# Optimization experiments

Measured on AMD Instinct MI355X. Metric: run time of the kernel, lower is better.

The kernel has to match this reference:

```python
import jax, jax.numpy as jnp
import numpy as np

NUM_LAYER = 6
NUM_HEADS = 1
NEG_INF = -1e9


def setup_inputs() -> dict:
    key = jax.random.key(0)
    ks = jax.random.split(key, 8)
    bs, C, N = 8, 128, 2048
    H0 = (jax.random.uniform(ks[0], (bs, N, N)) < 0.2).astype(jnp.float32)
    vertex_feat = jax.random.normal(ks[1], (bs, C, N), dtype=jnp.float32)
    edge_feat = jax.random.normal(ks[2], (bs, C, N), dtype=jnp.float32)
    s = 1.0 / np.sqrt(C)  # Conv1d(k=1) default init scale
    Wq = jax.random.uniform(ks[3], (C, C), minval=-s, maxval=s, dtype=jnp.float32)
    bq = jax.random.uniform(ks[4], (C,), minval=-s, maxval=s, dtype=jnp.float32)
    Wk = jax.random.uniform(ks[5], (C, C), minval=-s, maxval=s, dtype=jnp.float32)
    bk = jax.random.uniform(ks[6], (C,), minval=-s, maxval=s, dtype=jnp.float32)
    return {"H0": H0, "vertex_feat": vertex_feat, "edge_feat": edge_feat,
            "Wq": Wq, "bq": bq, "Wk": Wk, "bk": bk, "it": 4}


def reference(H0, vertex_feat, edge_feat, Wq, bq, Wk, bk, it):
    bs, N, _ = H0.shape
    C = Wq.shape[0]
    head = NUM_HEADS
    dh = C // head
    # Conv1d kernel_size=1 == pointwise linear over channel dim
    Q = (jnp.einsum('oc,bcn->bon', Wq, vertex_feat) + bq[None, :, None]).reshape(bs, head, dh, N)
    K = (jnp.einsum('oc,bcn->bon', Wk, edge_feat) + bk[None, :, None]).reshape(bs, head, dh, N)
    att = jnp.einsum('bhco,bhci->bhoi', Q, K) / np.sqrt(dh)  # [bs,h,N,N]
    mask = jnp.where(H0 > 0, 0.0, NEG_INF)                   # masked_fill(1-H0)
    score = jax.nn.sigmoid(att + mask[:, None]).sum(axis=1) / head  # [bs,N,N]
    # mask_score, choice='topk': keep top-k scores per row
    k = round(N * 0.1 * (NUM_LAYER - 1 - it))
    topk_vals = jax.lax.top_k(score, k)[0]          # [bs,N,k]
    a_min = topk_vals[..., -1:]                     # k-th largest per row
    W = jnp.where(score >= a_min, score, 0.0)
    H = jnp.where(W > 0, H0, 0.0)
    # degree-normalization matrices (diag_embed of 1/deg, inf -> 0)
    deg_E = H.sum(axis=1)   # [bs,N] edge degrees
    deg_V = H.sum(axis=2)   # [bs,N] vertex degrees
    De_n_1 = jax.vmap(jnp.diag)(jnp.where(deg_E != 0, 1.0 / deg_E, 0.0))
    Dv_n_1 = jax.vmap(jnp.diag)(jnp.where(deg_V != 0, 1.0 / deg_V, 0.0))
    # edge weights: L2-normalized column sums of W (F.normalize, eps=1e-12)
    W_edge = W.sum(axis=1)
    nrm = jnp.maximum(jnp.linalg.norm(W_edge, axis=1, keepdims=True), 1e-12)
    W_edge = (W_edge / nrm)[:, :, None]  # [bs,N,1]
    return H, W, De_n_1, Dv_n_1, W_edge
```

## Files before the change

kernel.cpp:

```cpp
#include <hip/hip_runtime.h>
#include <math.h>

#define NUM_LAYER 6

__global__ __launch_bounds__(256) void qk_gemm(
    const float* __restrict__ Wq, const float* __restrict__ bq,
    const float* __restrict__ vf,
    const float* __restrict__ Wk, const float* __restrict__ bk,
    const float* __restrict__ ef,
    float* __restrict__ Qout, float* __restrict__ Kout,
    int C, int N, int bs) {
  int which = (int)blockIdx.y >= bs;
  int b = (int)blockIdx.y - (which ? bs : 0);
  const float* Wm = which ? Wk : Wq;
  const float* bias = which ? bk : bq;
  const float* X = (which ? ef : vf) + (size_t)b * C * N;
  float* P = (which ? Kout : Qout) + (size_t)b * C * N;
  int n0 = blockIdx.x * 128;
  __shared__ float As[8][128];
  __shared__ float Xs[8][128];
  int t = threadIdx.x;
  int tx = t & 15, ty = t >> 4;
  int ao = t >> 1, ac = (t & 1) * 4;
  int lk = t >> 5, lj = (t & 31) * 4;
  float acc[8][8] = {};
  for (int c0 = 0; c0 < C; c0 += 8) {
    __syncthreads();
    float4 wv = *(const float4*)&Wm[(size_t)ao * C + c0 + ac];
    As[ac + 0][ao] = wv.x; As[ac + 1][ao] = wv.y;
    As[ac + 2][ao] = wv.z; As[ac + 3][ao] = wv.w;
    *(float4*)&Xs[lk][lj] = *(const float4*)&X[(size_t)(c0 + lk) * N + n0 + lj];
    __syncthreads();
#pragma unroll
    for (int kk = 0; kk < 8; ++kk) {
      float a[8], bb[8];
      *(float4*)&a[0]  = *(const float4*)&As[kk][ty * 4];
      *(float4*)&a[4]  = *(const float4*)&As[kk][64 + ty * 4];
      *(float4*)&bb[0] = *(const float4*)&Xs[kk][tx * 4];
      *(float4*)&bb[4] = *(const float4*)&Xs[kk][64 + tx * 4];
#pragma unroll
      for (int i = 0; i < 8; ++i)
#pragma unroll
        for (int j = 0; j < 8; ++j)
          acc[i][j] = fmaf(a[i], bb[j], acc[i][j]);
    }
  }
#pragma unroll
  for (int i = 0; i < 8; ++i) {
    int row = (i >> 2) * 64 + ty * 4 + (i & 3);
    float bv = bias[row];
    float4 o0 = { acc[i][0] + bv, acc[i][1] + bv, acc[i][2] + bv, acc[i][3] + bv };
    float4 o1 = { acc[i][4] + bv, acc[i][5] + bv, acc[i][6] + bv, acc[i][7] + bv };
    *(float4*)&P[(size_t)row * N + n0 + tx * 4] = o0;
    *(float4*)&P[(size_t)row * N + n0 + 64 + tx * 4] = o1;
  }
}

__global__ __launch_bounds__(256) void att_score(
    const float* __restrict__ Q, const float* __restrict__ K,
    const float* __restrict__ H0, float* __restrict__ score,
    int C, int N, float rsdh) {
  int b = blockIdx.z;
  int o0 = blockIdx.y * 128, i0 = blockIdx.x * 128;
  const float* Qb = Q + (size_t)b * C * N;
  const float* Kb = K + (size_t)b * C * N;
  const float* Hb = H0 + (size_t)b * N * N;
  float* Sb = score + (size_t)b * N * N;
  __shared__ float As[8][128];
  __shared__ float Bs[8][128];
  int t = threadIdx.x;
  int tx = t & 15, ty = t >> 4;
  int lk = t >> 5, lj = (t & 31) * 4;
  float acc[8][8] = {};
  for (int c0 = 0; c0 < C; c0 += 8) {
    __syncthreads();
    *(float4*)&As[lk][lj] = *(const float4*)&Qb[(size_t)(c0 + lk) * N + o0 + lj];
    *(float4*)&Bs[lk][lj] = *(const float4*)&Kb[(size_t)(c0 + lk) * N + i0 + lj];
    __syncthreads();
#pragma unroll
    for (int kk = 0; kk < 8; ++kk) {
      float a[8], bb[8];
      *(float4*)&a[0]  = *(const float4*)&As[kk][ty * 4];
      *(float4*)&a[4]  = *(const float4*)&As[kk][64 + ty * 4];
      *(float4*)&bb[0] = *(const float4*)&Bs[kk][tx * 4];
      *(float4*)&bb[4] = *(const float4*)&Bs[kk][64 + tx * 4];
#pragma unroll
      for (int i = 0; i < 8; ++i)
#pragma unroll
        for (int j = 0; j < 8; ++j)
          acc[i][j] = fmaf(a[i], bb[j], acc[i][j]);
    }
  }
#pragma unroll
  for (int i = 0; i < 8; ++i) {
    int row = o0 + (i >> 2) * 64 + ty * 4 + (i & 3);
    size_t base = (size_t)row * N + i0;
#pragma unroll
    for (int g = 0; g < 2; ++g) {
      size_t off = base + g * 64 + tx * 4;
      float4 h = *(const float4*)&Hb[off];
      float4 o;
      o.x = (h.x > 0.f) ? 1.f / (1.f + __expf(-acc[i][g*4+0] * rsdh)) : 0.f;
      o.y = (h.y > 0.f) ? 1.f / (1.f + __expf(-acc[i][g*4+1] * rsdh)) : 0.f;
      o.z = (h.z > 0.f) ? 1.f / (1.f + __expf(-acc[i][g*4+2] * rsdh)) : 0.f;
      o.w = (h.w > 0.f) ? 1.f / (1.f + __expf(-acc[i][g*4+3] * rsdh)) : 0.f;
      *(float4*)&Sb[off] = o;
    }
  }
}

template <int NQ>
__global__ __launch_bounds__(512) void select_wh_t(
    const float* __restrict__ H0, float* __restrict__ scoreW,
    float* __restrict__ Hout, float* __restrict__ degV,
    float* __restrict__ PE, float* __restrict__ PW,
    const int* __restrict__ itp, int N) {
  int b = blockIdx.y;
  int strip = blockIdx.x;
  int r0 = strip * 8;
  int t = threadIdx.x;
  int wave = t >> 6, lane = t & 63;
  size_t bNN = (size_t)b * N * N;
  __shared__ float aminS[8];
  __shared__ float dpart[8][8];

  {
    int row = r0 + wave;
    const float* srow = scoreW + bNN + (size_t)row * N;
    float v[NQ];
#pragma unroll
    for (int q = 0; q < NQ; ++q) v[q] = srow[lane + (q << 6)];
    int itv = *itp;
    int k = (int)floor((double)N * 0.1 * (double)(NUM_LAYER - 1 - itv) + 0.5);
    unsigned lo = 0u, hi = 0x3F800000u;
    while (lo < hi) {
      unsigned mid = lo + ((hi - lo + 1u) >> 1);
      float thr = __uint_as_float(mid);
      int c = 0;
#pragma unroll
      for (int q = 0; q < NQ; ++q) c += (v[q] >= thr) ? 1 : 0;
#pragma unroll
      for (int off = 1; off < 64; off <<= 1) c += __shfl_xor(c, off);
      if (c >= k) lo = mid; else hi = mid - 1u;
    }
    if (lane == 0) aminS[wave] = __uint_as_float(lo);
  }
  __syncthreads();

  float4 accE = {0.f, 0.f, 0.f, 0.f};
  float4 accW = {0.f, 0.f, 0.f, 0.f};
  float dv[8];
#pragma unroll
  for (int r = 0; r < 8; ++r) {
    float am = aminS[r];
    size_t off = bNN + (size_t)(r0 + r) * N + 4 * t;
    float4 s  = *(const float4*)(scoreW + off);
    float4 h0 = *(const float4*)(H0 + off);
    float4 w, h;
    w.x = (s.x >= am) ? s.x : 0.f; h.x = (w.x > 0.f) ? h0.x : 0.f;
    w.y = (s.y >= am) ? s.y : 0.f; h.y = (w.y > 0.f) ? h0.y : 0.f;
    w.z = (s.z >= am) ? s.z : 0.f; h.z = (w.z > 0.f) ? h0.z : 0.f;
    w.w = (s.w >= am) ? s.w : 0.f; h.w = (w.w > 0.f) ? h0.w : 0.f;
    *(float4*)(scoreW + off) = w;
    *(float4*)(Hout + off) = h;
    accW.x += w.x; accW.y += w.y; accW.z += w.z; accW.w += w.w;
    accE.x += h.x; accE.y += h.y; accE.z += h.z; accE.w += h.w;
    dv[r] = h.x + h.y + h.z + h.w;
  }
#pragma unroll
  for (int r = 0; r < 8; ++r) {
    float x = dv[r];
#pragma unroll
    for (int off = 32; off; off >>= 1) x += __shfl_down(x, off);
    if (lane == 0) dpart[wave][r] = x;
  }
  __syncthreads();
  if (t < 8) {
    float s = 0.f;
#pragma unroll
    for (int w = 0; w < 8; ++w) s += dpart[w][t];
    degV[b * N + r0 + t] = s;
  }
  int S = N >> 3;
  size_t pbase = ((size_t)b * S + strip) * N + 4 * t;
  *(float4*)(PE + pbase) = accE;
  *(float4*)(PW + pbase) = accW;
}

__global__ __launch_bounds__(256) void col_reduce(
    const float* __restrict__ PE, const float* __restrict__ PW,
    float* __restrict__ degE, float* __restrict__ We, int N, int S) {
  int b = blockIdx.y;
  int col = blockIdx.x * 256 + threadIdx.x;
  float se = 0.f, sw = 0.f;
  for (int s = 0; s < S; ++s) {
    size_t off = ((size_t)b * S + s) * N + col;
    se += PE[off];
    sw += PW[off];
  }
  degE[b * N + col] = se;
  We[b * N + col] = sw;
}

__global__ __launch_bounds__(256) void diag_write(
    float* __restrict__ De, float* __restrict__ Dv,
    const float* __restrict__ degE, const float* __restrict__ degV, int N) {
  int idx = blockIdx.x * 256 + threadIdx.x;
  int b = idx / N, i = idx - b * N;
  size_t d = (size_t)b * N * N + (size_t)i * N + i;
  float e = degE[idx], v = degV[idx];
  De[d] = (e != 0.f) ? 1.f / e : 0.f;
  Dv[d] = (v != 0.f) ? 1.f / v : 0.f;
}

__global__ __launch_bounds__(256) void wedge_norm(
    const float* __restrict__ We, float* __restrict__ out, int N) {
  int b = blockIdx.x;
  int t = threadIdx.x;
  const float* w = We + (size_t)b * N;
  float ss = 0.f;
  for (int i = t; i < N; i += 256) { float x = w[i]; ss += x * x; }
  for (int off = 32; off; off >>= 1) ss += __shfl_down(ss, off);
  __shared__ float p[4];
  if ((t & 63) == 0) p[t >> 6] = ss;
  __syncthreads();
  float tot = p[0] + p[1] + p[2] + p[3];
  float nrm = fmaxf(sqrtf(tot), 1e-12f);
  for (int i = t; i < N; i += 256) out[(size_t)b * N + i] = w[i] / nrm;
}

extern "C" void kernel_launch(void* const* d_in, const int* in_sizes, int n_in,
                              void* d_out, int out_size, void* d_ws, size_t ws_size,
                              hipStream_t stream) {
  const float* H0 = (const float*)d_in[0];
  const float* vf = (const float*)d_in[1];
  const float* ef = (const float*)d_in[2];
  const float* Wq = (const float*)d_in[3];
  const float* bq = (const float*)d_in[4];
  const float* Wk = (const float*)d_in[5];
  const float* bk = (const float*)d_in[6];
  const int* itp  = (const int*)d_in[7];

  int C = (int)(sqrt((double)in_sizes[3]) + 0.5);
  long long ratio = (long long)in_sizes[0] / in_sizes[1];
  int N = (int)(C * ratio);
  int bs = (int)(in_sizes[1] / ((long long)C * N));
  size_t bNN = (size_t)bs * N * N;
  size_t bCN = (size_t)bs * C * N;
  int S = N >> 3;
  size_t pElems = (size_t)bs * S * N;

  float* outH  = (float*)d_out;
  float* outW  = outH + bNN;
  float* outDe = outW + bNN;
  float* outDv = outDe + bNN;
  float* outWe = outDv + bNN;

  size_t bsN = (size_t)bs * N;
  float* degE = (float*)d_ws;
  float* degV = degE + bsN;
  float* We   = degV + bsN;
  float* Q;
  float* K;
  float* PE;
  float* PW;
  size_t need = (3 * bsN + 2 * bCN + 2 * pElems) * sizeof(float);
  if (ws_size >= need) {
    Q  = We + bsN;
    K  = Q + bCN;
    PE = K + bCN;
    PW = PE + pElems;
  } else {
    Q  = outDe;
    K  = Q + bCN;
    PE = outDv;
    PW = PE + pElems;
  }

  float rsdh = (float)(1.0 / sqrt((double)C));

  qk_gemm<<<dim3(N / 128, 2 * bs), 256, 0, stream>>>(Wq, bq, vf, Wk, bk, ef,
                                                     Q, K, C, N, bs);
  att_score<<<dim3(N / 128, N / 128, bs), 256, 0, stream>>>(Q, K, H0, outW,
                                                            C, N, rsdh);
  if (N == 2048)
    select_wh_t<32><<<dim3(S, bs), 512, 0, stream>>>(H0, outW, outH, degV,
                                                     PE, PW, itp, N);
  else if (N == 1024)
    select_wh_t<16><<<dim3(S, bs), 512, 0, stream>>>(H0, outW, outH, degV,
                                                     PE, PW, itp, N);
  else
    select_wh_t<64><<<dim3(S, bs), 512, 0, stream>>>(H0, outW, outH, degV,
                                                     PE, PW, itp, N);
  col_reduce<<<dim3(N / 256, bs), 256, 0, stream>>>(PE, PW, degE, We, N, S);
  hipMemsetAsync(outDe, 0, 2 * bNN * sizeof(float), stream);
  diag_write<<<dim3((bs * N) / 256), 256, 0, stream>>>(outDe, outDv, degE,
                                                       degV, N);
  wedge_norm<<<dim3(bs), 256, 0, stream>>>(We, outWe, N);
}
```

Measured before the change: 936.4 us.

## Compute attention scores on bf16 MFMA with three-way split emulation of fp32

The Q/K projection now writes each value as three bf16 parts (high, mid, low) in an N-major layout. The attention GEMM runs on MFMA 16x16x32 bf16 instructions, using six cross-products to recover close to fp32 accuracy. This replaces the scalar FP32 FMA GEMM with matrix-core throughput at the cost of six times the MFMA work and extra split traffic. The masked-sigmoid epilogue now does scalar loads and stores per element instead of float4, which may lose coalescing.

```diff
diff --git a/kernel.cpp b/kernel.cpp
--- a/kernel.cpp
+++ b/kernel.cpp
@@ -3,19 +3,36 @@
 
 #define NUM_LAYER 6
 
-__global__ __launch_bounds__(256) void qk_gemm(
+typedef __attribute__((ext_vector_type(8))) short short8;
+typedef __attribute__((ext_vector_type(4))) float f32x4;
+typedef unsigned short u16;
+
+__device__ __forceinline__ void split3(float x, u16& h, u16& m, u16& l) {
+  unsigned ux = __float_as_uint(x);
+  h = (u16)(ux >> 16);
+  float r1 = x - __uint_as_float(ux & 0xFFFF0000u);
+  unsigned u1 = __float_as_uint(r1);
+  m = (u16)(u1 >> 16);
+  float r2 = r1 - __uint_as_float(u1 & 0xFFFF0000u);
+  l = (u16)(__float_as_uint(r2) >> 16);
+}
+
+__global__ __launch_bounds__(256) void qk_gemm_split(
     const float* __restrict__ Wq, const float* __restrict__ bq,
     const float* __restrict__ vf,
     const float* __restrict__ Wk, const float* __restrict__ bk,
     const float* __restrict__ ef,
-    float* __restrict__ Qout, float* __restrict__ Kout,
+    u16* __restrict__ Qh, u16* __restrict__ Qm, u16* __restrict__ Ql,
+    u16* __restrict__ Kh, u16* __restrict__ Km, u16* __restrict__ Kl,
     int C, int N, int bs) {
   int which = (int)blockIdx.y >= bs;
   int b = (int)blockIdx.y - (which ? bs : 0);
   const float* Wm = which ? Wk : Wq;
   const float* bias = which ? bk : bq;
   const float* X = (which ? ef : vf) + (size_t)b * C * N;
-  float* P = (which ? Kout : Qout) + (size_t)b * C * N;
+  u16* Ph = which ? Kh : Qh;
+  u16* Pm = which ? Km : Qm;
+  u16* Pl = which ? Kl : Ql;
   int n0 = blockIdx.x * 128;
   __shared__ float As[8][128];
   __shared__ float Xs[8][128];
@@ -45,66 +62,106 @@
           acc[i][j] = fmaf(a[i], bb[j], acc[i][j]);
     }
   }
-#pragma unroll
-  for (int i = 0; i < 8; ++i) {
-    int row = (i >> 2) * 64 + ty * 4 + (i & 3);
-    float bv = bias[row];
-    float4 o0 = { acc[i][0] + bv, acc[i][1] + bv, acc[i][2] + bv, acc[i][3] + bv };
-    float4 o1 = { acc[i][4] + bv, acc[i][5] + bv, acc[i][6] + bv, acc[i][7] + bv };
-    *(float4*)&P[(size_t)row * N + n0 + tx * 4] = o0;
-    *(float4*)&P[(size_t)row * N + n0 + 64 + tx * 4] = o1;
-  }
-}
-
-__global__ __launch_bounds__(256) void att_score(
-    const float* __restrict__ Q, const float* __restrict__ K,
+  float bv[8];
+#pragma unroll
+  for (int i = 0; i < 8; ++i) bv[i] = bias[(i >> 2) * 64 + ty * 4 + (i & 3)];
+#pragma unroll
+  for (int j = 0; j < 8; ++j) {
+    int n = n0 + tx * 4 + (j & 3) + (j >> 2) * 64;
+    size_t nb = ((size_t)b * N + n) * C;
+#pragma unroll
+    for (int g = 0; g < 2; ++g) {
+      int r0 = g * 64 + ty * 4;
+      ushort4 hv, mv, lv;
+      split3(acc[g * 4 + 0][j] + bv[g * 4 + 0], hv.x, mv.x, lv.x);
+      split3(acc[g * 4 + 1][j] + bv[g * 4 + 1], hv.y, mv.y, lv.y);
+      split3(acc[g * 4 + 2][j] + bv[g * 4 + 2], hv.z, mv.z, lv.z);
+      split3(acc[g * 4 + 3][j] + bv[g * 4 + 3], hv.w, mv.w, lv.w);
+      *(ushort4*)&Ph[nb + r0] = hv;
+      *(ushort4*)&Pm[nb + r0] = mv;
+      *(ushort4*)&Pl[nb + r0] = lv;
+    }
+  }
+}
+
+__global__ __launch_bounds__(256) void att_mfma(
+    const u16* __restrict__ Qh, const u16* __restrict__ Qm,
+    const u16* __restrict__ Ql, const u16* __restrict__ Kh,
+    const u16* __restrict__ Km, const u16* __restrict__ Kl,
     const float* __restrict__ H0, float* __restrict__ score,
     int C, int N, float rsdh) {
   int b = blockIdx.z;
   int o0 = blockIdx.y * 128, i0 = blockIdx.x * 128;
-  const float* Qb = Q + (size_t)b * C * N;
-  const float* Kb = K + (size_t)b * C * N;
+  __shared__ u16 sm[6][128][40];
+  int t = threadIdx.x;
+  int wave = t >> 6, lane = t & 63, quad = lane >> 4, lr = lane & 15;
+  int wo = wave >> 1, wi = wave & 1;
+  f32x4 acc[4][4];
+#pragma unroll
+  for (int mi = 0; mi < 4; ++mi)
+#pragma unroll
+    for (int ni = 0; ni < 4; ++ni) acc[mi][ni] = (f32x4){0.f, 0.f, 0.f, 0.f};
+
+  int ro = t >> 1, ch = (t & 1) * 16;
+  size_t qbase = ((size_t)b * N + o0 + ro) * C + ch;
+  size_t kbase = ((size_t)b * N + i0 + ro) * C + ch;
+  const u16* gq[3] = {Qh, Qm, Ql};
+  const u16* gk[3] = {Kh, Km, Kl};
+
+  for (int c0 = 0; c0 < C; c0 += 32) {
+    __syncthreads();
+#pragma unroll
+    for (int a = 0; a < 3; ++a) {
+      const uint4* src = (const uint4*)(gq[a] + qbase + c0);
+      *(uint4*)&sm[a][ro][ch] = src[0];
+      *(uint4*)&sm[a][ro][ch + 8] = src[1];
+      const uint4* srk = (const uint4*)(gk[a] + kbase + c0);
+      *(uint4*)&sm[3 + a][ro][ch] = srk[0];
+      *(uint4*)&sm[3 + a][ro][ch + 8] = srk[1];
+    }
+    __syncthreads();
+    short8 bh[4], bm[4], bl[4];
+#pragma unroll
+    for (int ni = 0; ni < 4; ++ni) {
+      int row = wi * 64 + ni * 16 + lr;
+      bh[ni] = *(const short8*)&sm[3][row][quad * 8];
+      bm[ni] = *(const short8*)&sm[4][row][quad * 8];
+      bl[ni] = *(const short8*)&sm[5][row][quad * 8];
+    }
+#pragma unroll
+    for (int mi = 0; mi < 4; ++mi) {
+      int row = wo * 64 + mi * 16 + lr;
+      short8 ah = *(const short8*)&sm[0][row][quad * 8];
+      short8 am = *(const short8*)&sm[1][row][quad * 8];
+      short8 al = *(const short8*)&sm[2][row][quad * 8];
+#pragma unroll
+      for (int ni = 0; ni < 4; ++ni) {
+        f32x4 c = acc[mi][ni];
+        c = __builtin_amdgcn_mfma_f32_16x16x32_bf16(ah, bl[ni], c, 0, 0, 0);
+        c = __builtin_amdgcn_mfma_f32_16x16x32_bf16(al, bh[ni], c, 0, 0, 0);
+        c = __builtin_amdgcn_mfma_f32_16x16x32_bf16(am, bm[ni], c, 0, 0, 0);
+        c = __builtin_amdgcn_mfma_f32_16x16x32_bf16(ah, bm[ni], c, 0, 0, 0);
+        c = __builtin_amdgcn_mfma_f32_16x16x32_bf16(am, bh[ni], c, 0, 0, 0);
+        c = __builtin_amdgcn_mfma_f32_16x16x32_bf16(ah, bh[ni], c, 0, 0, 0);
+        acc[mi][ni] = c;
+      }
+    }
+  }
   const float* Hb = H0 + (size_t)b * N * N;
   float* Sb = score + (size_t)b * N * N;
-  __shared__ float As[8][128];
-  __shared__ float Bs[8][128];
-  int t = threadIdx.x;
-  int tx = t & 15, ty = t >> 4;
-  int lk = t >> 5, lj = (t & 31) * 4;
-  float acc[8][8] = {};
-  for (int c0 = 0; c0 < C; c0 += 8) {
-    __syncthreads();
-    *(float4*)&As[lk][lj] = *(const float4*)&Qb[(size_t)(c0 + lk) * N + o0 + lj];
-    *(float4*)&Bs[lk][lj] = *(const float4*)&Kb[(size_t)(c0 + lk) * N + i0 + lj];
-    __syncthreads();
-#pragma unroll
-    for (int kk = 0; kk < 8; ++kk) {
-      float a[8], bb[8];
-      *(float4*)&a[0]  = *(const float4*)&As[kk][ty * 4];
-      *(float4*)&a[4]  = *(const float4*)&As[kk][64 + ty * 4];
-      *(float4*)&bb[0] = *(const float4*)&Bs[kk][tx * 4];
-      *(float4*)&bb[4] = *(const float4*)&Bs[kk][64 + tx * 4];
-#pragma unroll
-      for (int i = 0; i < 8; ++i)
-#pragma unroll
-        for (int j = 0; j < 8; ++j)
-          acc[i][j] = fmaf(a[i], bb[j], acc[i][j]);
-    }
-  }
-#pragma unroll
-  for (int i = 0; i < 8; ++i) {
-    int row = o0 + (i >> 2) * 64 + ty * 4 + (i & 3);
-    size_t base = (size_t)row * N + i0;
-#pragma unroll
-    for (int g = 0; g < 2; ++g) {
-      size_t off = base + g * 64 + tx * 4;
-      float4 h = *(const float4*)&Hb[off];
-      float4 o;
-      o.x = (h.x > 0.f) ? 1.f / (1.f + __expf(-acc[i][g*4+0] * rsdh)) : 0.f;
-      o.y = (h.y > 0.f) ? 1.f / (1.f + __expf(-acc[i][g*4+1] * rsdh)) : 0.f;
-      o.z = (h.z > 0.f) ? 1.f / (1.f + __expf(-acc[i][g*4+2] * rsdh)) : 0.f;
-      o.w = (h.w > 0.f) ? 1.f / (1.f + __expf(-acc[i][g*4+3] * rsdh)) : 0.f;
-      *(float4*)&Sb[off] = o;
+#pragma unroll
+  for (int mi = 0; mi < 4; ++mi) {
+    int o = o0 + wo * 64 + mi * 16 + quad * 4;
+#pragma unroll
+    for (int ni = 0; ni < 4; ++ni) {
+      int i = i0 + wi * 64 + ni * 16 + lr;
+#pragma unroll
+      for (int r = 0; r < 4; ++r) {
+        size_t idx = (size_t)(o + r) * N + i;
+        float h0 = Hb[idx];
+        float a = acc[mi][ni][r] * rsdh;
+        Sb[idx] = (h0 > 0.f) ? 1.f / (1.f + __expf(-a)) : 0.f;
+      }
     }
   }
 }
@@ -246,7 +303,7 @@
   int N = (int)(C * ratio);
   int bs = (int)(in_sizes[1] / ((long long)C * N));
   size_t bNN = (size_t)bs * N * N;
-  size_t bCN = (size_t)bs * C * N;
+  size_t bNC = (size_t)bs * N * C;
   int S = N >> 3;
   size_t pElems = (size_t)bs * S * N;
 
@@ -260,29 +317,33 @@
   float* degE = (float*)d_ws;
   float* degV = degE + bsN;
   float* We   = degV + bsN;
-  float* Q;
-  float* K;
+  u16* splits;
   float* PE;
   float* PW;
-  size_t need = (3 * bsN + 2 * bCN + 2 * pElems) * sizeof(float);
+  size_t need = 3 * bsN * sizeof(float) + 6 * bNC * sizeof(u16) +
+                2 * pElems * sizeof(float);
   if (ws_size >= need) {
-    Q  = We + bsN;
-    K  = Q + bCN;
-    PE = K + bCN;
+    splits = (u16*)(We + bsN);
+    PE = (float*)(splits + 6 * bNC);
     PW = PE + pElems;
   } else {
-    Q  = outDe;
-    K  = Q + bCN;
+    splits = (u16*)outDe;
     PE = outDv;
     PW = PE + pElems;
   }
+  u16* Qh = splits;
+  u16* Qm = Qh + bNC;
+  u16* Ql = Qm + bNC;
+  u16* Kh = Ql + bNC;
+  u16* Km = Kh + bNC;
+  u16* Kl = Km + bNC;
 
   float rsdh = (float)(1.0 / sqrt((double)C));
 
-  qk_gemm<<<dim3(N / 128, 2 * bs), 256, 0, stream>>>(Wq, bq, vf, Wk, bk, ef,
-                                                     Q, K, C, N, bs);
-  att_score<<<dim3(N / 128, N / 128, bs), 256, 0, stream>>>(Q, K, H0, outW,
-                                                            C, N, rsdh);
+  qk_gemm_split<<<dim3(N / 128, 2 * bs), 256, 0, stream>>>(
+      Wq, bq, vf, Wk, bk, ef, Qh, Qm, Ql, Kh, Km, Kl, C, N, bs);
+  att_mfma<<<dim3(N / 128, N / 128, bs), 256, 0, stream>>>(
+      Qh, Qm, Ql, Kh, Km, Kl, H0, outW, C, N, rsdh);
   if (N == 2048)
     select_wh_t<32><<<dim3(S, bs), 512, 0, stream>>>(H0, outW, outH, degV,
                                                      PE, PW, itp, N);
```

New measurement: 1.048 ms. 11.9% more time.
